# Performance work log

Hardware: AMD Instinct MI355X
Metric: run time of the kernel (lower is better)

## Reference

```python
import jax, jax.numpy as jnp
import numpy as np

B, S, H = 2, 2048, 2048
NH = 16
HD = H // NH  # 128


def setup_inputs() -> dict:
    key = jax.random.key(0)
    ks = jax.random.split(key, 5)
    scale = 1.0 / np.sqrt(H)
    return {
        "hidden_states": jax.random.normal(ks[0], (B, S, H), dtype=jnp.float32),
        "attention_mask": jnp.zeros((B, 1, S, S), dtype=jnp.float32),
        "q_weight": jax.random.normal(ks[1], (H, H), dtype=jnp.float32) * scale,
        "k_weight": jax.random.normal(ks[2], (H, H), dtype=jnp.float32) * scale,
        "v_weight": jax.random.normal(ks[3], (H, H), dtype=jnp.float32) * scale,
        "o_weight": jax.random.normal(ks[4], (H, H), dtype=jnp.float32) * scale,
    }


def reference(hidden_states, attention_mask, q_weight, k_weight, v_weight, o_weight):
    b, s, h = hidden_states.shape
    # Linear(y = x @ W.T), then split heads: [b, nh, s, hd]
    q = (hidden_states @ q_weight.T).reshape(b, s, NH, HD).transpose(0, 2, 1, 3)
    k = (hidden_states @ k_weight.T).reshape(b, s, NH, HD).transpose(0, 2, 1, 3)
    v = (hidden_states @ v_weight.T).reshape(b, s, NH, HD).transpose(0, 2, 1, 3)
    scores = jnp.einsum("bhqd,bhkd->bhqk", q, k) / jnp.sqrt(jnp.float32(HD))
    scores = scores + attention_mask  # additive mask, broadcasts over heads
    attn = jax.nn.softmax(scores, axis=-1)
    out = jnp.einsum("bhqk,bhkd->bhqd", attn, v)
    out = out.transpose(0, 2, 1, 3).reshape(b, s, h)
    return out @ o_weight.T
```

## Files before the change

### kernel.cpp

```cpp
#include <hip/hip_runtime.h>
#include <stdint.h>

constexpr int SEQ   = 2048;
constexpr int NHEAD = 16;
constexpr int HDSZ  = 128;
constexpr int HDIM  = 2048;
constexpr float QK_SCALE = 0.08838834764831845f;

typedef __attribute__((ext_vector_type(8))) __bf16 bf16x8;
typedef __attribute__((ext_vector_type(4))) __bf16 bf16x4;
typedef __attribute__((ext_vector_type(2))) __bf16 bf16x2;
typedef __attribute__((ext_vector_type(4))) float  f32x4;

__device__ __forceinline__ void gl_lds16(const void* gptr, void* lptr) {
  __builtin_amdgcn_global_load_lds(
      (const __attribute__((address_space(1))) unsigned int*)gptr,
      (__attribute__((address_space(3))) unsigned int*)lptr, 16, 0, 0);
}

__global__ __launch_bounds__(256) void cast_f32_bf16(
    const float* __restrict__ in, __bf16* __restrict__ out, int n4) {
  int i = blockIdx.x * blockDim.x + threadIdx.x;
  int stride = gridDim.x * blockDim.x;
  for (; i < n4; i += stride) {
    float4 v = ((const float4*)in)[i];
    bf16x4 o = { (__bf16)v.x, (__bf16)v.y, (__bf16)v.z, (__bf16)v.w };
    ((bf16x4*)out)[i] = o;
  }
}

__global__ __launch_bounds__(256) void cast4_f32_bf16(
    const float* __restrict__ w0, const float* __restrict__ w1,
    const float* __restrict__ w2, const float* __restrict__ w3,
    __bf16* __restrict__ out, int n4) {
  const int y = blockIdx.y;
  const float* src = (y == 0) ? w0 : (y == 1) ? w1 : (y == 2) ? w2 : w3;
  __bf16* dst = out + (size_t)y * (size_t)n4 * 4;
  int i = blockIdx.x * blockDim.x + threadIdx.x;
  int stride = gridDim.x * blockDim.x;
  for (; i < n4; i += stride) {
    float4 v = ((const float4*)src)[i];
    bf16x4 o = { (__bf16)v.x, (__bf16)v.y, (__bf16)v.z, (__bf16)v.w };
    ((bf16x4*)dst)[i] = o;
  }
}

__global__ __launch_bounds__(256) void gemm_qkv(
    const __bf16* __restrict__ A, const __bf16* __restrict__ W,
    __bf16* __restrict__ qkv) {
  constexpr long XN = 4096L * 2048;
  constexpr int K = 2048;
  __shared__ __align__(16) char smem[64 * 136 * 2];
  __bf16* As = (__bf16*)smem;
  __bf16* Bs = As + 128 * 32;
  __bf16* Ts = (__bf16*)smem;

  const int tid  = threadIdx.x;
  const int lane = tid & 63;
  const int w    = tid >> 6;
  const int lg   = lane >> 4, lr = lane & 15;
  const int wr   = w >> 1, wc = w & 1;
  const int flat = blockIdx.y * 48 + blockIdx.x;
  const int swz  = (flat & 7) * 192 + (flat >> 3);
  const int mtile = swz & 31, ntile = swz >> 5;
  const long mbase = (long)mtile * 128;
  const long nbase = (long)ntile * 128;

  f32x4 acc[4][4];
#pragma unroll
  for (int i = 0; i < 4; ++i)
#pragma unroll
    for (int j = 0; j < 4; ++j) acc[i][j] = (f32x4){0.f, 0.f, 0.f, 0.f};

  const int srow = lane >> 2;
  const int scol = (lane & 3) * 8;

  for (int kt = 0; kt < K; kt += 32) {
#pragma unroll
    for (int i = 0; i < 2; ++i) {
      const int c = w * 2 + i;
      gl_lds16(A + (mbase + c * 16 + srow) * (long)K + kt + scol, &As[c * 512]);
      gl_lds16(W + (nbase + c * 16 + srow) * (long)K + kt + scol, &Bs[c * 512]);
    }
    __syncthreads();
    bf16x8 af[4], bfv[4];
#pragma unroll
    for (int mm = 0; mm < 4; ++mm)
      af[mm] = *(const bf16x8*)&As[(wr * 64 + mm * 16 + lr) * 32 + lg * 8];
#pragma unroll
    for (int nn = 0; nn < 4; ++nn)
      bfv[nn] = *(const bf16x8*)&Bs[(wc * 64 + nn * 16 + lr) * 32 + lg * 8];
    __builtin_amdgcn_s_setprio(1);
#pragma unroll
    for (int nn = 0; nn < 4; ++nn)
#pragma unroll
      for (int mm = 0; mm < 4; ++mm)
        acc[mm][nn] = __builtin_amdgcn_mfma_f32_16x16x32_bf16(
            af[mm], bfv[nn], acc[mm][nn], 0, 0, 0);
    __builtin_amdgcn_s_setprio(0);
    __syncthreads();
  }

  const int  mat = ntile >> 4;
  const long nb2 = nbase - (long)mat * 2048;
  const long b   = mbase >> 11, s0 = mbase & 2047;
  const long h   = nb2 >> 7;

  if (mat < 2) {
    __bf16* out = qkv + (size_t)mat * XN;
#pragma unroll
    for (int dh = 0; dh < 2; ++dh) {
      if (wr == dh) {
#pragma unroll
        for (int mm = 0; mm < 4; ++mm)
#pragma unroll
          for (int nn = 0; nn < 4; ++nn) {
            const int d = wc * 64 + nn * 16 + lr;
#pragma unroll
            for (int r = 0; r < 4; ++r)
              Ts[(mm * 16 + lg * 4 + r) * 136 + d] = (__bf16)acc[mm][nn][r];
          }
      }
      __syncthreads();
#pragma unroll
      for (int it = 0; it < 4; ++it) {
        const int idx = it * 256 + tid;
        const int row = idx >> 4, c = idx & 15;
        bf16x8 v = *(const bf16x8*)&Ts[row * 136 + c * 8];
        *(bf16x8*)&out[((b * NHEAD + h) * SEQ + s0 + dh * 64 + row) * HDSZ +
                       c * 8] = v;
      }
      __syncthreads();
    }
  } else {
    __bf16* out = qkv + 2 * XN;
#pragma unroll
    for (int dh = 0; dh < 2; ++dh) {
      if (wc == dh) {
#pragma unroll
        for (int mm = 0; mm < 4; ++mm)
#pragma unroll
          for (int nn = 0; nn < 4; ++nn) {
            const int dd = nn * 16 + lr;
            bf16x4 pk = { (__bf16)acc[mm][nn][0], (__bf16)acc[mm][nn][1],
                          (__bf16)acc[mm][nn][2], (__bf16)acc[mm][nn][3] };
            *(bf16x4*)&Ts[dd * 136 + wr * 64 + mm * 16 + lg * 4] = pk;
          }
      }
      __syncthreads();
#pragma unroll
      for (int it = 0; it < 4; ++it) {
        const int idx = it * 256 + tid;
        const int dd = idx >> 4, c = idx & 15;
        bf16x8 v = *(const bf16x8*)&Ts[dd * 136 + c * 8];
        *(bf16x8*)&out[((b * NHEAD + h) * HDSZ + dh * 64 + dd) * SEQ +
                       s0 + c * 8] = v;
      }
      __syncthreads();
    }
  }
}

__global__ __launch_bounds__(256) void gemm_bt_f32(
    const __bf16* __restrict__ A, const __bf16* __restrict__ B,
    float* __restrict__ C, int M, int N, int K) {
  __shared__ __bf16 As[128 * 32];
  __shared__ __bf16 Bs[128 * 32];
  const int tid  = threadIdx.x;
  const int lane = tid & 63;
  const int w    = tid >> 6;
  const int lg   = lane >> 4, lr = lane & 15;
  const int wr   = w >> 1, wc = w & 1;
  const int flat = blockIdx.y * 16 + blockIdx.x;
  const int swz  = (flat & 7) * 64 + (flat >> 3);
  const long mbase = (long)(swz >> 4) * 128;
  const long nbase = (long)(swz & 15) * 128;

  f32x4 acc[4][4];
#pragma unroll
  for (int i = 0; i < 4; ++i)
#pragma unroll
    for (int j = 0; j < 4; ++j) acc[i][j] = (f32x4){0.f, 0.f, 0.f, 0.f};

  const int srow = lane >> 2;
  const int scol = (lane & 3) * 8;

  for (int kt = 0; kt < K; kt += 32) {
#pragma unroll
    for (int i = 0; i < 2; ++i) {
      const int c = w * 2 + i;
      gl_lds16(A + (mbase + c * 16 + srow) * (long)K + kt + scol, &As[c * 512]);
      gl_lds16(B + (nbase + c * 16 + srow) * (long)K + kt + scol, &Bs[c * 512]);
    }
    __syncthreads();
    bf16x8 af[4], bfv[4];
#pragma unroll
    for (int mm = 0; mm < 4; ++mm)
      af[mm] = *(const bf16x8*)&As[(wr * 64 + mm * 16 + lr) * 32 + lg * 8];
#pragma unroll
    for (int nn = 0; nn < 4; ++nn)
      bfv[nn] = *(const bf16x8*)&Bs[(wc * 64 + nn * 16 + lr) * 32 + lg * 8];
    __builtin_amdgcn_s_setprio(1);
#pragma unroll
    for (int nn = 0; nn < 4; ++nn)
#pragma unroll
      for (int mm = 0; mm < 4; ++mm)
        acc[mm][nn] = __builtin_amdgcn_mfma_f32_16x16x32_bf16(
            af[mm], bfv[nn], acc[mm][nn], 0, 0, 0);
    __builtin_amdgcn_s_setprio(0);
    __syncthreads();
  }

#pragma unroll
  for (int mm = 0; mm < 4; ++mm)
#pragma unroll
    for (int nn = 0; nn < 4; ++nn) {
      const long n = nbase + wc * 64 + nn * 16 + lr;
#pragma unroll
      for (int r = 0; r < 4; ++r) {
        const long m = mbase + wr * 64 + mm * 16 + lg * 4 + r;
        C[m * (long)N + n] = acc[mm][nn][r];
      }
    }
}

__global__ __launch_bounds__(512, 4) void attn_fused(
    const __bf16* __restrict__ Q, const __bf16* __restrict__ K,
    const __bf16* __restrict__ Vt, const float* __restrict__ mask,
    __bf16* __restrict__ Out) {
  __shared__ __bf16 Ks[2 * 64 * 128];
  __shared__ __bf16 Vs[2 * 128 * 64];
  __shared__ __bf16 Ps[128 * 64];

  const int tid  = threadIdx.x;
  const int lane = tid & 63;
  const int w    = tid >> 6;
  const int lg   = lane >> 4, lr = lane & 15;
  const int flat = blockIdx.y * 16 + blockIdx.x;
  const int swz  = (flat & 7) * 64 + (flat >> 3);
  const int bh   = swz >> 4;
  const int b    = bh >> 4, h = bh & 15;
  const int q0   = (swz & 15) * 128;

  const __bf16* Qh = Q  + (size_t)bh * SEQ * HDSZ;
  const __bf16* Kh = K  + (size_t)bh * SEQ * HDSZ;
  const __bf16* Vh = Vt + (size_t)bh * HDSZ * SEQ;
  const float*  Mb = mask + (size_t)b * SEQ * SEQ;

  bf16x8 qf[4];
#pragma unroll
  for (int kk = 0; kk < 4; ++kk)
    qf[kk] = *(const bf16x8*)(
        Qh + (size_t)(q0 + w * 16 + lr) * HDSZ + kk * 32 + lg * 8);

  const __bf16* ksrc[2];
  const __bf16* vsrc[2];
#pragma unroll
  for (int i = 0; i < 2; ++i) {
    const int ch = i * 512 + tid;
    const int krow = ch >> 4, kc = ch & 15;
    ksrc[i] = Kh + (size_t)krow * HDSZ + (((kc & 8) | ((kc ^ krow) & 7)) * 8);
    const int vrow = ch >> 3, vc = ch & 7;
    vsrc[i] = Vh + (size_t)vrow * SEQ + (((vc ^ vrow) & 7) * 8);
  }

  float mrw = -1e30f, lrw = 0.f;
  f32x4 acco[8];
#pragma unroll
  for (int n = 0; n < 8; ++n) acco[n] = (f32x4){0.f, 0.f, 0.f, 0.f};

#pragma unroll
  for (int i = 0; i < 2; ++i) {
    gl_lds16(ksrc[i], &Ks[(i * 512 + w * 64) * 8]);
    gl_lds16(vsrc[i], &Vs[(i * 512 + w * 64) * 8]);
  }
  __syncthreads();

  constexpr int NT = SEQ / 64;
  for (int t = 0; t < NT; ++t) {
    const int cur = t & 1;
    const int kt = t * 64;
    const char* Kb = (const char*)(Ks + cur * (64 * 128));
    const char* Vb = (const char*)(Vs + cur * (128 * 64));

    f32x4 mk[4];
#pragma unroll
    for (int n = 0; n < 4; ++n)
      mk[n] = *(const f32x4*)(
          Mb + (size_t)(q0 + w * 16 + lr) * SEQ + kt + n * 16 + lg * 4);
    __builtin_amdgcn_sched_barrier(0);

    if (t + 1 < NT) {
      const int nk = kt + 64;
      __bf16* Kn = Ks + (cur ^ 1) * (64 * 128);
      __bf16* Vn = Vs + (cur ^ 1) * (128 * 64);
#pragma unroll
      for (int i = 0; i < 2; ++i) {
        gl_lds16(ksrc[i] + (size_t)nk * HDSZ, &Kn[(i * 512 + w * 64) * 8]);
        gl_lds16(vsrc[i] + nk, &Vn[(i * 512 + w * 64) * 8]);
      }
    }
    __builtin_amdgcn_sched_barrier(0);

    f32x4 sacc[4];
#pragma unroll
    for (int n = 0; n < 4; ++n) sacc[n] = (f32x4){0.f, 0.f, 0.f, 0.f};
    __builtin_amdgcn_s_setprio(1);
#pragma unroll
    for (int n = 0; n < 4; ++n)
#pragma unroll
      for (int kk = 0; kk < 4; ++kk) {
        const int cp = (kk * 4 + lg) ^ (lr & 7);
        bf16x8 kf = *(const bf16x8*)(Kb + ((n * 16 + lr) << 8) + (cp << 4));
        sacc[n] = __builtin_amdgcn_mfma_f32_16x16x32_bf16(kf, qf[kk], sacc[n], 0, 0, 0);
      }
    __builtin_amdgcn_s_setprio(0);

    float sv[4][4];
    float tm = -1e30f;
#pragma unroll
    for (int n = 0; n < 4; ++n)
#pragma unroll
      for (int r = 0; r < 4; ++r) {
        float x = fmaf(sacc[n][r], QK_SCALE, mk[n][r]);
        sv[n][r] = x;
        tm = fmaxf(tm, x);
      }
    tm = fmaxf(tm, __shfl_xor(tm, 16));
    tm = fmaxf(tm, __shfl_xor(tm, 32));
    const float mn = fmaxf(mrw, tm);
    const float corr = __expf(mrw - mn);
    mrw = mn;
    float ls = 0.f;
#pragma unroll
    for (int n = 0; n < 4; ++n)
#pragma unroll
      for (int r = 0; r < 4; ++r) {
        float p = __expf(sv[n][r] - mn);
        sv[n][r] = p;
        ls += p;
      }
    ls += __shfl_xor(ls, 16);
    ls += __shfl_xor(ls, 32);
    lrw = lrw * corr + ls;
    float cb[4];
#pragma unroll
    for (int r = 0; r < 4; ++r) cb[r] = __shfl(corr, lg * 4 + r);
#pragma unroll
    for (int n = 0; n < 8; ++n)
#pragma unroll
      for (int r = 0; r < 4; ++r) acco[n][r] *= cb[r];

#pragma unroll
    for (int n = 0; n < 4; ++n)
#pragma unroll
      for (int rp = 0; rp < 2; ++rp) {
        bf16x2 pk = { (__bf16)sv[n][2 * rp], (__bf16)sv[n][2 * rp + 1] };
        const int pbyte = (n * 32 + lg * 8 + rp * 4) ^ ((lr & 7) << 4);
        *(bf16x2*)((char*)Ps + (w * 16 + lr) * 128 + pbyte) = pk;
      }
    __asm__ volatile("s_waitcnt lgkmcnt(0)" ::: "memory");
    __builtin_amdgcn_sched_barrier(0);

    __builtin_amdgcn_s_setprio(1);
#pragma unroll
    for (int kk = 0; kk < 2; ++kk) {
      const int pcp = (kk * 4 + lg) ^ (lr & 7);
      bf16x8 pa = *(const bf16x8*)(
          (const char*)Ps + (w * 16 + lr) * 128 + (pcp << 4));
#pragma unroll
      for (int n = 0; n < 8; ++n) {
        const int cp = (kk * 4 + lg) ^ (lr & 7);
        bf16x8 vf = *(const bf16x8*)(Vb + ((n * 16 + lr) << 7) + (cp << 4));
        acco[n] = __builtin_amdgcn_mfma_f32_16x16x32_bf16(pa, vf, acco[n], 0, 0, 0);
      }
    }
    __builtin_amdgcn_s_setprio(0);

    __syncthreads();
  }

  float lb[4];
#pragma unroll
  for (int r = 0; r < 4; ++r) lb[r] = __shfl(lrw, lg * 4 + r);
#pragma unroll
  for (int r = 0; r < 4; ++r) {
    const float inv = 1.0f / lb[r];
    const int srow = q0 + w * 16 + lg * 4 + r;
    const size_t base = ((size_t)b * SEQ + srow) * HDIM + h * HDSZ;
#pragma unroll
    for (int n = 0; n < 8; ++n)
      Out[base + n * 16 + lr] = (__bf16)(acco[n][r] * inv);
  }
}

extern "C" void kernel_launch(void* const* d_in, const int* in_sizes, int n_in,
                              void* d_out, int out_size, void* d_ws, size_t ws_size,
                              hipStream_t stream) {
  const float* x    = (const float*)d_in[0];
  const float* mask = (const float*)d_in[1];
  const float* wq   = (const float*)d_in[2];
  const float* wk   = (const float*)d_in[3];
  const float* wv   = (const float*)d_in[4];
  const float* wo   = (const float*)d_in[5];

  constexpr long XN = 4096L * 2048;
  constexpr long WN = 2048L * 2048;

  __bf16* xbf = (__bf16*)d_ws;
  __bf16* wqb = xbf + XN;
  __bf16* wob = wqb + 3 * WN;
  __bf16* qw  = wqb + 4 * WN;
  __bf16* kw  = qw + XN;
  __bf16* vtw = kw + XN;
  __bf16* aw  = vtw + XN;

  cast_f32_bf16<<<2048, 256, 0, stream>>>(x, xbf, (int)(XN / 4));
  cast4_f32_bf16<<<dim3(256, 4), 256, 0, stream>>>(wq, wk, wv, wo, wqb,
                                                   (int)(WN / 4));

  gemm_qkv<<<dim3(48, 32), 256, 0, stream>>>(xbf, wqb, qw);

  attn_fused<<<dim3(16, 32), 512, 0, stream>>>(qw, kw, vtw, mask, aw);

  gemm_bt_f32<<<dim3(16, 32), 256, 0, stream>>>(aw, wob, (float*)d_out,
                                                4096, 2048, 2048);
}
```

Measured before the change: 335.8 us.

## Double-buffer LDS tiles in QKV and output-projection GEMMs

```diff
diff --git a/kernel.cpp b/kernel.cpp
--- a/kernel.cpp
+++ b/kernel.cpp
@@ -50,9 +50,7 @@
     __bf16* __restrict__ qkv) {
   constexpr long XN = 4096L * 2048;
   constexpr int K = 2048;
-  __shared__ __align__(16) char smem[64 * 136 * 2];
-  __bf16* As = (__bf16*)smem;
-  __bf16* Bs = As + 128 * 32;
+  __shared__ __align__(16) char smem[2 * 16384];
   __bf16* Ts = (__bf16*)smem;
 
   const int tid  = threadIdx.x;
@@ -75,14 +73,27 @@
   const int srow = lane >> 2;
   const int scol = (lane & 3) * 8;
 
-  for (int kt = 0; kt < K; kt += 32) {
+  auto stage = [&](int buf, int kt) {
+    __bf16* As = (__bf16*)(smem + buf * 16384);
+    __bf16* Bs = As + 128 * 32;
 #pragma unroll
     for (int i = 0; i < 2; ++i) {
       const int c = w * 2 + i;
       gl_lds16(A + (mbase + c * 16 + srow) * (long)K + kt + scol, &As[c * 512]);
       gl_lds16(W + (nbase + c * 16 + srow) * (long)K + kt + scol, &Bs[c * 512]);
     }
-    __syncthreads();
+  };
+
+  stage(0, 0);
+  __syncthreads();
+
+  constexpr int NTK = K / 32;
+  for (int t = 0; t < NTK; ++t) {
+    const int cur = t & 1;
+    if (t + 1 < NTK) stage(cur ^ 1, (t + 1) * 32);
+    __builtin_amdgcn_sched_barrier(0);
+    const __bf16* As = (const __bf16*)(smem + cur * 16384);
+    const __bf16* Bs = As + 128 * 32;
     bf16x8 af[4], bfv[4];
 #pragma unroll
     for (int mm = 0; mm < 4; ++mm)
@@ -164,8 +175,7 @@
 __global__ __launch_bounds__(256) void gemm_bt_f32(
     const __bf16* __restrict__ A, const __bf16* __restrict__ B,
     float* __restrict__ C, int M, int N, int K) {
-  __shared__ __bf16 As[128 * 32];
-  __shared__ __bf16 Bs[128 * 32];
+  __shared__ __align__(16) char smem[2 * 16384];
   const int tid  = threadIdx.x;
   const int lane = tid & 63;
   const int w    = tid >> 6;
@@ -185,14 +195,27 @@
   const int srow = lane >> 2;
   const int scol = (lane & 3) * 8;
 
-  for (int kt = 0; kt < K; kt += 32) {
+  auto stage = [&](int buf, int kt) {
+    __bf16* As = (__bf16*)(smem + buf * 16384);
+    __bf16* Bs = As + 128 * 32;
 #pragma unroll
     for (int i = 0; i < 2; ++i) {
       const int c = w * 2 + i;
       gl_lds16(A + (mbase + c * 16 + srow) * (long)K + kt + scol, &As[c * 512]);
       gl_lds16(B + (nbase + c * 16 + srow) * (long)K + kt + scol, &Bs[c * 512]);
     }
-    __syncthreads();
+  };
+
+  stage(0, 0);
+  __syncthreads();
+
+  const int NTK = K / 32;
+  for (int t = 0; t < NTK; ++t) {
+    const int cur = t & 1;
+    if (t + 1 < NTK) stage(cur ^ 1, (t + 1) * 32);
+    __builtin_amdgcn_sched_barrier(0);
+    const __bf16* As = (const __bf16*)(smem + cur * 16384);
+    const __bf16* Bs = As + 128 * 32;
     bf16x8 af[4], bfv[4];
 #pragma unroll
     for (int mm = 0; mm < 4; ++mm)
```

Result: faster. 326.4 us (-2.8%).

## Double-buffer GEMM LDS tiles with K=64 steps and XOR-swizzled layout

Applied to the files above, without the earlier changes.

```diff
diff --git a/kernel.cpp b/kernel.cpp
--- a/kernel.cpp
+++ b/kernel.cpp
@@ -50,10 +50,12 @@
     __bf16* __restrict__ qkv) {
   constexpr long XN = 4096L * 2048;
   constexpr int K = 2048;
-  __shared__ __align__(16) char smem[64 * 136 * 2];
-  __bf16* As = (__bf16*)smem;
-  __bf16* Bs = As + 128 * 32;
-  __bf16* Ts = (__bf16*)smem;
+  __shared__ __align__(16) char smem[4 * 16384];
+  __bf16* const As0 = (__bf16*)(smem);
+  __bf16* const Bs0 = (__bf16*)(smem + 16384);
+  __bf16* const As1 = (__bf16*)(smem + 32768);
+  __bf16* const Bs1 = (__bf16*)(smem + 49152);
+  __bf16* const Ts  = (__bf16*)(smem);
 
   const int tid  = threadIdx.x;
   const int lane = tid & 63;
@@ -72,34 +74,68 @@
 #pragma unroll
     for (int j = 0; j < 4; ++j) acc[i][j] = (f32x4){0.f, 0.f, 0.f, 0.f};
 
-  const int srow = lane >> 2;
-  const int scol = (lane & 3) * 8;
-
-  for (int kt = 0; kt < K; kt += 32) {
-#pragma unroll
-    for (int i = 0; i < 2; ++i) {
-      const int c = w * 2 + i;
-      gl_lds16(A + (mbase + c * 16 + srow) * (long)K + kt + scol, &As[c * 512]);
-      gl_lds16(W + (nbase + c * 16 + srow) * (long)K + kt + scol, &Bs[c * 512]);
-    }
+  const __bf16* asrc[4];
+  const __bf16* wsrc[4];
+#pragma unroll
+  for (int i = 0; i < 4; ++i) {
+    const int row = w * 32 + i * 8 + (lane >> 3);
+    const int cs  = ((lane & 7) ^ (row & 7)) * 8;
+    asrc[i] = A + (mbase + row) * (long)K + cs;
+    wsrc[i] = W + (nbase + row) * (long)K + cs;
+  }
+
+  auto stageto = [&](__bf16* As, __bf16* Bs, int ko) {
+#pragma unroll
+    for (int i = 0; i < 4; ++i) {
+      gl_lds16(asrc[i] + ko, &As[(w * 32 + i * 8) * 64]);
+      gl_lds16(wsrc[i] + ko, &Bs[(w * 32 + i * 8) * 64]);
+    }
+  };
+  auto computeb = [&](const __bf16* As, const __bf16* Bs) {
+#pragma unroll
+    for (int kk = 0; kk < 2; ++kk) {
+      const int cp = ((kk * 4 + lg) ^ (lr & 7)) << 4;
+      bf16x8 af[4], bfv[4];
+#pragma unroll
+      for (int mm = 0; mm < 4; ++mm)
+        af[mm] = *(const bf16x8*)(
+            (const char*)As + (wr * 64 + mm * 16 + lr) * 128 + cp);
+#pragma unroll
+      for (int nn = 0; nn < 4; ++nn)
+        bfv[nn] = *(const bf16x8*)(
+            (const char*)Bs + (wc * 64 + nn * 16 + lr) * 128 + cp);
+      __builtin_amdgcn_s_setprio(1);
+#pragma unroll
+      for (int nn = 0; nn < 4; ++nn)
+#pragma unroll
+        for (int mm = 0; mm < 4; ++mm)
+          acc[mm][nn] = __builtin_amdgcn_mfma_f32_16x16x32_bf16(
+              af[mm], bfv[nn], acc[mm][nn], 0, 0, 0);
+      __builtin_amdgcn_s_setprio(0);
+    }
+  };
+
+  stageto(As0, Bs0, 0);
+  __syncthreads();
+
+  int ko = 64;
+  for (int tp = 0; tp < 15; ++tp) {
+    stageto(As1, Bs1, ko);
+    __builtin_amdgcn_sched_barrier(0);
+    computeb(As0, Bs0);
     __syncthreads();
-    bf16x8 af[4], bfv[4];
-#pragma unroll
-    for (int mm = 0; mm < 4; ++mm)
-      af[mm] = *(const bf16x8*)&As[(wr * 64 + mm * 16 + lr) * 32 + lg * 8];
-#pragma unroll
-    for (int nn = 0; nn < 4; ++nn)
-      bfv[nn] = *(const bf16x8*)&Bs[(wc * 64 + nn * 16 + lr) * 32 + lg * 8];
-    __builtin_amdgcn_s_setprio(1);
-#pragma unroll
-    for (int nn = 0; nn < 4; ++nn)
-#pragma unroll
-      for (int mm = 0; mm < 4; ++mm)
-        acc[mm][nn] = __builtin_amdgcn_mfma_f32_16x16x32_bf16(
-            af[mm], bfv[nn], acc[mm][nn], 0, 0, 0);
-    __builtin_amdgcn_s_setprio(0);
+    stageto(As0, Bs0, ko + 64);
+    __builtin_amdgcn_sched_barrier(0);
+    computeb(As1, Bs1);
     __syncthreads();
-  }
+    ko += 128;
+  }
+  stageto(As1, Bs1, ko);
+  __builtin_amdgcn_sched_barrier(0);
+  computeb(As0, Bs0);
+  __syncthreads();
+  computeb(As1, Bs1);
+  __syncthreads();
 
   const int  mat = ntile >> 4;
   const long nb2 = nbase - (long)mat * 2048;
@@ -164,8 +200,12 @@
 __global__ __launch_bounds__(256) void gemm_bt_f32(
     const __bf16* __restrict__ A, const __bf16* __restrict__ B,
     float* __restrict__ C, int M, int N, int K) {
-  __shared__ __bf16 As[128 * 32];
-  __shared__ __bf16 Bs[128 * 32];
+  __shared__ __align__(16) char smem[4 * 16384];
+  __bf16* const As0 = (__bf16*)(smem);
+  __bf16* const Bs0 = (__bf16*)(smem + 16384);
+  __bf16* const As1 = (__bf16*)(smem + 32768);
+  __bf16* const Bs1 = (__bf16*)(smem + 49152);
+
   const int tid  = threadIdx.x;
   const int lane = tid & 63;
   const int w    = tid >> 6;
@@ -182,34 +222,67 @@
 #pragma unroll
     for (int j = 0; j < 4; ++j) acc[i][j] = (f32x4){0.f, 0.f, 0.f, 0.f};
 
-  const int srow = lane >> 2;
-  const int scol = (lane & 3) * 8;
-
-  for (int kt = 0; kt < K; kt += 32) {
-#pragma unroll
-    for (int i = 0; i < 2; ++i) {
-      const int c = w * 2 + i;
-      gl_lds16(A + (mbase + c * 16 + srow) * (long)K + kt + scol, &As[c * 512]);
-      gl_lds16(B + (nbase + c * 16 + srow) * (long)K + kt + scol, &Bs[c * 512]);
-    }
+  const __bf16* asrc[4];
+  const __bf16* bsrc[4];
+#pragma unroll
+  for (int i = 0; i < 4; ++i) {
+    const int row = w * 32 + i * 8 + (lane >> 3);
+    const int cs  = ((lane & 7) ^ (row & 7)) * 8;
+    asrc[i] = A + (mbase + row) * (long)K + cs;
+    bsrc[i] = B + (nbase + row) * (long)K + cs;
+  }
+
+  auto stageto = [&](__bf16* As, __bf16* Bs, int ko) {
+#pragma unroll
+    for (int i = 0; i < 4; ++i) {
+      gl_lds16(asrc[i] + ko, &As[(w * 32 + i * 8) * 64]);
+      gl_lds16(bsrc[i] + ko, &Bs[(w * 32 + i * 8) * 64]);
+    }
+  };
+  auto computeb = [&](const __bf16* As, const __bf16* Bs) {
+#pragma unroll
+    for (int kk = 0; kk < 2; ++kk) {
+      const int cp = ((kk * 4 + lg) ^ (lr & 7)) << 4;
+      bf16x8 af[4], bfv[4];
+#pragma unroll
+      for (int mm = 0; mm < 4; ++mm)
+        af[mm] = *(const bf16x8*)(
+            (const char*)As + (wr * 64 + mm * 16 + lr) * 128 + cp);
+#pragma unroll
+      for (int nn = 0; nn < 4; ++nn)
+        bfv[nn] = *(const bf16x8*)(
+            (const char*)Bs + (wc * 64 + nn * 16 + lr) * 128 + cp);
+      __builtin_amdgcn_s_setprio(1);
+#pragma unroll
+      for (int nn = 0; nn < 4; ++nn)
+#pragma unroll
+        for (int mm = 0; mm < 4; ++mm)
+          acc[mm][nn] = __builtin_amdgcn_mfma_f32_16x16x32_bf16(
+              af[mm], bfv[nn], acc[mm][nn], 0, 0, 0);
+      __builtin_amdgcn_s_setprio(0);
+    }
+  };
+
+  stageto(As0, Bs0, 0);
+  __syncthreads();
+
+  int ko = 64;
+  for (int tp = 0; tp < 15; ++tp) {
+    stageto(As1, Bs1, ko);
+    __builtin_amdgcn_sched_barrier(0);
+    computeb(As0, Bs0);
     __syncthreads();
-    bf16x8 af[4], bfv[4];
-#pragma unroll
-    for (int mm = 0; mm < 4; ++mm)
-      af[mm] = *(const bf16x8*)&As[(wr * 64 + mm * 16 + lr) * 32 + lg * 8];
-#pragma unroll
-    for (int nn = 0; nn < 4; ++nn)
-      bfv[nn] = *(const bf16x8*)&Bs[(wc * 64 + nn * 16 + lr) * 32 + lg * 8];
-    __builtin_amdgcn_s_setprio(1);
-#pragma unroll
-    for (int nn = 0; nn < 4; ++nn)
-#pragma unroll
-      for (int mm = 0; mm < 4; ++mm)
-        acc[mm][nn] = __builtin_amdgcn_mfma_f32_16x16x32_bf16(
-            af[mm], bfv[nn], acc[mm][nn], 0, 0, 0);
-    __builtin_amdgcn_s_setprio(0);
+    stageto(As0, Bs0, ko + 64);
+    __builtin_amdgcn_sched_barrier(0);
+    computeb(As1, Bs1);
     __syncthreads();
-  }
+    ko += 128;
+  }
+  stageto(As1, Bs1, ko);
+  __builtin_amdgcn_sched_barrier(0);
+  computeb(As0, Bs0);
+  __syncthreads();
+  computeb(As1, Bs1);
 
 #pragma unroll
   for (int mm = 0; mm < 4; ++mm)
```

Measured after the change: 296.7 us. 1.13x faster.
